# Kernel tuning notes

Measured on AMD Instinct MI355X. Metric: run time of the kernel, lower is better.

## Reference

```python
import jax, jax.numpy as jnp
import numpy as np

N = 50000      # nodes
E = 800000     # edges (avg degree 16)
G = 1024       # graphs in batch
C = 128        # hidden / interaction channels
FIN = 16       # num_node_features
FE = 3         # num_edge_features
L = 3          # num_interactions
CUTOFF = 10.0
LOG2 = float(np.log(2.0))
BN_EPS = 1e-5

def ssp(v):
    # ShiftedSoftplus: softplus(x) - log(2)
    return jax.nn.softplus(v) - LOG2

def setup_inputs() -> dict:
    key = jax.random.key(0)
    ks = jax.random.split(key, 24)
    s = 0.05
    inp = {}
    inp["x"] = jax.random.normal(ks[0], (N, FIN), jnp.float32)
    inp["edge_index"] = jax.random.randint(ks[1], (2, E), 0, N, dtype=jnp.int32)
    inp["edge_weight"] = jax.random.uniform(ks[2], (E,), jnp.float32) * CUTOFF
    inp["edge_attr"] = jax.random.normal(ks[3], (E, FE), jnp.float32)
    inp["batch"] = jnp.sort(jax.random.randint(ks[4], (N,), 0, G, dtype=jnp.int32))
    # node embedding (node_data='x'): Linear(FIN,C) -> Linear(C,C)
    inp["W_l1"] = jax.random.normal(ks[5], (FIN, C), jnp.float32) * s
    inp["b_l1"] = jnp.zeros((C,), jnp.float32)
    inp["W_l2"] = jax.random.normal(ks[6], (C, C), jnp.float32) * s
    inp["b_l2"] = jnp.zeros((C,), jnp.float32)
    # BatchNorm1d affine params
    inp["bn_g"] = jnp.ones((C,), jnp.float32)
    inp["bn_b"] = jnp.zeros((C,), jnp.float32)
    # L stacked interaction layers (SchNet-style CFConv)
    inp["Wi_in"] = jax.random.normal(ks[7], (L, C, C), jnp.float32) * s
    inp["bi_in"] = jnp.zeros((L, C), jnp.float32)
    inp["We1"] = jax.random.normal(ks[8], (L, FE, C), jnp.float32) * s
    inp["be1"] = jnp.zeros((L, C), jnp.float32)
    inp["We2"] = jax.random.normal(ks[9], (L, C, C), jnp.float32) * s
    inp["be2"] = jnp.zeros((L, C), jnp.float32)
    inp["Wi_out"] = jax.random.normal(ks[10], (L, C, C), jnp.float32) * s
    inp["bi_out"] = jnp.zeros((L, C), jnp.float32)
    # GeneralReadOutLayer (128,'sum',32,1): pool -> Linear(128,32)+SSP -> Linear(32,1)+SSP
    inp["W_r1"] = jax.random.normal(ks[11], (C, 32), jnp.float32) * s
    inp["b_r1"] = jnp.zeros((32,), jnp.float32)
    inp["W_r2"] = jax.random.normal(ks[12], (32, 1), jnp.float32) * s
    inp["b_r2"] = jnp.zeros((1,), jnp.float32)
    return inp

def _forward(x, edge_weight, edge_attr,
             W_l1, b_l1, W_l2, b_l2, bn_g, bn_b,
             Wi_in, bi_in, We1, be1, We2, be2, Wi_out, bi_out,
             W_r1, b_r1, W_r2, b_r2, edge_index, batch):
    src, dst = edge_index[0], edge_index[1]
    # node embedding: Linear -> Linear
    h = (x @ W_l1 + b_l1) @ W_l2 + b_l2                   # [N, C]
    # BatchNorm1d (training-mode batch stats over nodes)
    mu = jnp.mean(h, axis=0)
    var = jnp.var(h, axis=0)
    h = (h - mu) * jax.lax.rsqrt(var + BN_EPS) * bn_g + bn_b
    # cosine cutoff envelope on edge distances
    env = 0.5 * (jnp.cos(edge_weight * (jnp.pi / CUTOFF)) + 1.0)  # [E]
    # GeoResNet: residual stack of interactions
    for i in range(L):
        filt = ssp(edge_attr @ We1[i] + be1[i]) @ We2[i] + be2[i]   # [E, C]
        hin = h @ Wi_in[i] + bi_in[i]                               # [N, C]
        msg = hin[src] * filt * env[:, None]                        # [E, C] gather
        agg = jax.ops.segment_sum(msg, dst, num_segments=N)         # [N, C] scatter
        h = h + ssp(agg @ Wi_out[i] + bi_out[i])
    # GeneralReadOutLayer: segment 'sum' pool then MLP with SSP
    hg = jax.ops.segment_sum(h, batch, num_segments=G)              # [G, C]
    out = ssp(hg @ W_r1 + b_r1)
    out = ssp(out @ W_r2 + b_r2)                                    # [G, 1]
    return out.reshape(-1)                                          # [G]

def reference(x, edge_index, edge_weight, edge_attr, batch,
              W_l1, b_l1, W_l2, b_l2, bn_g, bn_b,
              Wi_in, bi_in, We1, be1, We2, be2, Wi_out, bi_out,
              W_r1, b_r1, W_r2, b_r2):
    return _forward(x, edge_weight, edge_attr,
                    W_l1, b_l1, W_l2, b_l2, bn_g, bn_b,
                    Wi_in, bi_in, We1, be1, We2, be2, Wi_out, bi_out,
                    W_r1, b_r1, W_r2, b_r2, edge_index, batch)
```

## Files before the change

kernel.cpp:

```cpp
#include <hip/hip_runtime.h>
#include <hip/hip_bf16.h>
#include <math.h>

#define N_NODES 50000
#define N_EDGES 800000
#define N_GRAPH 1024
#define CDIM 128
#define FINDIM 16
#define NL 3
#define WTP 132
#define NSCB 196

using short8  = __attribute__((ext_vector_type(8))) short;
using floatx4 = __attribute__((ext_vector_type(4))) float;

__device__ __forceinline__ float sspf(float x) {
    return __logf(1.0f + __expf(x)) - 0.6931471805599453f;
}

__device__ __forceinline__ unsigned short f2bf(float f) {
    unsigned int u = __float_as_uint(f);
    u = u + 0x7FFFu + ((u >> 16) & 1u);
    return (unsigned short)(u >> 16);
}

__device__ __forceinline__ float bf2f(unsigned short h) {
    return __uint_as_float((unsigned int)h << 16);
}

__device__ __forceinline__ unsigned int packbf(float a, float b) {
    __hip_bfloat162 h = __float22bfloat162_rn(make_float2(a, b));
    return *(unsigned int*)&h;
}

__device__ __forceinline__ short8 ldfrag(const unsigned short* T, int row, int k0) {
    const uint2* p = (const uint2*)(T + row * WTP + k0);
    short8 r;
    *(uint2*)&r       = p[0];
    *((uint2*)&r + 1) = p[1];
    return r;
}

__global__ void k_fuse(const float* __restrict__ Wl1, const float* __restrict__ bl1,
                       const float* __restrict__ Wl2, const float* __restrict__ bl2,
                       float* __restrict__ Wf, float* __restrict__ bfv) {
    int o = blockIdx.x * 256 + threadIdx.x;
    if (o < FINDIM * CDIM) {
        int f = o >> 7, c = o & 127;
        float s = 0.f;
#pragma unroll 4
        for (int k = 0; k < CDIM; ++k) s += Wl1[f * CDIM + k] * Wl2[k * CDIM + c];
        Wf[o] = s;
    } else if (o < FINDIM * CDIM + CDIM) {
        int c = o - FINDIM * CDIM;
        float s = bl2[c];
#pragma unroll 4
        for (int k = 0; k < CDIM; ++k) s += bl1[k] * Wl2[k * CDIM + c];
        bfv[c] = s;
    }
}

__global__ void k_embed_bn(const float* __restrict__ x, const float* __restrict__ Wf,
                           const float* __restrict__ bfv, float* __restrict__ h,
                           float* __restrict__ bnsum) {
    __shared__ float wfs[FINDIM * CDIM];
    __shared__ float bfs[CDIM];
    __shared__ float sd[512];
    for (int o = threadIdx.x; o < FINDIM * CDIM; o += 256) wfs[o] = Wf[o];
    if (threadIdx.x < CDIM) bfs[threadIdx.x] = bfv[threadIdx.x];
    __syncthreads();
    int c = threadIdx.x & 127;
    int half = threadIdx.x >> 7;
    float s1 = 0.f, s2 = 0.f;
    for (int base = blockIdx.x * 2; base < N_NODES; base += gridDim.x * 2) {
        int n = base + half;
        if (n < N_NODES) {
            float s = bfs[c];
            const float* xp = x + (size_t)n * FINDIM;
#pragma unroll
            for (int f = 0; f < FINDIM; ++f) s += xp[f] * wfs[f * CDIM + c];
            h[(size_t)n * CDIM + c] = s;
            s1 += s; s2 += s * s;
        }
    }
    sd[threadIdx.x] = s1; sd[256 + threadIdx.x] = s2;
    __syncthreads();
    if (threadIdx.x < 128) {
        atomicAdd(&bnsum[threadIdx.x], sd[threadIdx.x] + sd[threadIdx.x + 128]);
        atomicAdd(&bnsum[128 + threadIdx.x], sd[256 + threadIdx.x] + sd[256 + threadIdx.x + 128]);
    }
}

__global__ void k_hist(const int* __restrict__ edst, int* __restrict__ deg) {
    int e = blockIdx.x * 256 + threadIdx.x;
    if (e < N_EDGES) atomicAdd(&deg[edst[e]], 1);
}

__global__ void k_scan1(const int* __restrict__ deg, int* __restrict__ bsum) {
    __shared__ int sd[256];
    int i = blockIdx.x * 256 + threadIdx.x;
    sd[threadIdx.x] = (i < N_NODES) ? deg[i] : 0;
    __syncthreads();
    for (int off = 128; off > 0; off >>= 1) {
        if (threadIdx.x < off) sd[threadIdx.x] += sd[threadIdx.x + off];
        __syncthreads();
    }
    if (threadIdx.x == 0) bsum[blockIdx.x] = sd[0];
}

__global__ void k_scan2(const int* __restrict__ bsum, int* __restrict__ boff,
                        int* __restrict__ row_ptr) {
    __shared__ int sd[256];
    int t = threadIdx.x;
    int v = (t < NSCB) ? bsum[t] : 0;
    sd[t] = v;
    __syncthreads();
    for (int off = 1; off < 256; off <<= 1) {
        int u = (t >= off) ? sd[t - off] : 0;
        __syncthreads();
        sd[t] += u;
        __syncthreads();
    }
    if (t < NSCB) boff[t] = sd[t] - v;
    if (t == 255) row_ptr[N_NODES] = sd[255];
}

__global__ void k_scan3(const int* __restrict__ deg, const int* __restrict__ boff,
                        int* __restrict__ row_ptr) {
    __shared__ int sd[256];
    int i = blockIdx.x * 256 + threadIdx.x;
    int t = threadIdx.x;
    int v = (i < N_NODES) ? deg[i] : 0;
    sd[t] = v;
    __syncthreads();
    for (int off = 1; off < 256; off <<= 1) {
        int u = (t >= off) ? sd[t - off] : 0;
        __syncthreads();
        sd[t] += u;
        __syncthreads();
    }
    if (i < N_NODES) row_ptr[i] = boff[blockIdx.x] + sd[t] - v;
}

__global__ void k_scatter_pack(const int* __restrict__ esrc, const int* __restrict__ edst,
                               const float* __restrict__ ew, const float* __restrict__ ea,
                               const int* __restrict__ row_ptr, int* __restrict__ cnt,
                               int2* __restrict__ rmeta, float4* __restrict__ rea) {
    int e = blockIdx.x * 256 + threadIdx.x;
    if (e < N_EDGES) {
        int d = edst[e];
        int pos = row_ptr[d] + atomicAdd(&cnt[d], 1);
        rmeta[pos] = make_int2(esrc[e], d);
        float w = ew[e];
        float env = 0.5f * (__cosf(w * 0.31415926535897932f) + 1.0f);
        rea[pos] = make_float4(ea[(size_t)e * 3], ea[(size_t)e * 3 + 1],
                               ea[(size_t)e * 3 + 2], env);
    }
}

__global__ __launch_bounds__(256, 2) void k_ngemm_in_bn(float* __restrict__ h,
                                                        const float* __restrict__ bnsum,
                                                        const float* __restrict__ g,
                                                        const float* __restrict__ b,
                                                        const float* __restrict__ B,
                                                        const float* __restrict__ bias,
                                                        unsigned short* __restrict__ hinb) {
    __shared__ unsigned short WT[128 * WTP];
    __shared__ float bs[CDIM];
    __shared__ float scale[CDIM];
    __shared__ float shift[CDIM];
    for (int o = threadIdx.x; o < CDIM * CDIM; o += 256) {
        int k = o >> 7, c = o & 127;
        WT[c * WTP + k] = f2bf(B[o]);
    }
    if (threadIdx.x < CDIM) {
        int c = threadIdx.x;
        const float invN = 1.0f / (float)N_NODES;
        float mu  = bnsum[c] * invN;
        float var = bnsum[128 + c] * invN - mu * mu;
        float sc  = g[c] * rsqrtf(var + 1e-5f);
        scale[c] = sc;
        shift[c] = b[c] - mu * sc;
        bs[c] = bias[c];
    }
    __syncthreads();

    int lane = threadIdx.x & 63, wave = threadIdx.x >> 6;
    int m = lane & 15, q = lane >> 4;
    int rb = blockIdx.x * 64 + wave * 16;
    bool rowok = (rb + m) < N_NODES;
    int row = rowok ? (rb + m) : (N_NODES - 1);

    floatx4 acc[8];
#pragma unroll
    for (int nt = 0; nt < 8; ++nt) acc[nt] = (floatx4){0.f, 0.f, 0.f, 0.f};

#pragma unroll
    for (int kb = 0; kb < 4; ++kb) {
        int k0 = kb * 32 + q * 8;
        float* ap = h + (size_t)row * CDIM + k0;
        float4 lo = *(const float4*)ap;
        float4 hi = *(const float4*)(ap + 4);
        lo.x = fmaf(lo.x, scale[k0 + 0], shift[k0 + 0]);
        lo.y = fmaf(lo.y, scale[k0 + 1], shift[k0 + 1]);
        lo.z = fmaf(lo.z, scale[k0 + 2], shift[k0 + 2]);
        lo.w = fmaf(lo.w, scale[k0 + 3], shift[k0 + 3]);
        hi.x = fmaf(hi.x, scale[k0 + 4], shift[k0 + 4]);
        hi.y = fmaf(hi.y, scale[k0 + 5], shift[k0 + 5]);
        hi.z = fmaf(hi.z, scale[k0 + 6], shift[k0 + 6]);
        hi.w = fmaf(hi.w, scale[k0 + 7], shift[k0 + 7]);
        if (rowok) { *(float4*)ap = lo; *(float4*)(ap + 4) = hi; }
        short8 af;
        ((unsigned int*)&af)[0] = packbf(lo.x, lo.y);
        ((unsigned int*)&af)[1] = packbf(lo.z, lo.w);
        ((unsigned int*)&af)[2] = packbf(hi.x, hi.y);
        ((unsigned int*)&af)[3] = packbf(hi.z, hi.w);
#pragma unroll
        for (int nt = 0; nt < 8; ++nt) {
            short8 bf = ldfrag(WT, nt * 16 + m, k0);
            acc[nt] = __builtin_amdgcn_mfma_f32_16x16x32_bf16(af, bf, acc[nt], 0, 0, 0);
        }
    }
#pragma unroll
    for (int nt = 0; nt < 8; ++nt) {
        int c = nt * 16 + m;
#pragma unroll
        for (int r = 0; r < 4; ++r) {
            int orow = rb + q * 4 + r;
            if (orow < N_NODES)
                hinb[(size_t)orow * CDIM + c] = f2bf(acc[nt][r] + bs[c]);
        }
    }
}

__global__ __launch_bounds__(256, 2) void k_fused_oi(float* __restrict__ agg,
                                                     const float* __restrict__ Bo,
                                                     const float* __restrict__ bo,
                                                     float* __restrict__ h,
                                                     const float* __restrict__ Bi,
                                                     const float* __restrict__ bi,
                                                     unsigned short* __restrict__ hinb) {
    __shared__ unsigned short WT[128 * WTP];
    __shared__ unsigned short hnS[64 * WTP];
    __shared__ float bso[CDIM];
    __shared__ float bsi[CDIM];

    for (int o = threadIdx.x; o < CDIM * CDIM; o += 256) {
        int k = o >> 7, c = o & 127;
        WT[c * WTP + k] = f2bf(Bo[o]);
    }
    if (threadIdx.x < CDIM) { bso[threadIdx.x] = bo[threadIdx.x]; bsi[threadIdx.x] = bi[threadIdx.x]; }
    __syncthreads();

    int lane = threadIdx.x & 63, wave = threadIdx.x >> 6;
    int m = lane & 15, q = lane >> 4;
    int rb = blockIdx.x * 64 + wave * 16;
    int row = rb + m;
    if (row > N_NODES - 1) row = N_NODES - 1;

    floatx4 acc[8];
#pragma unroll
    for (int nt = 0; nt < 8; ++nt) acc[nt] = (floatx4){0.f, 0.f, 0.f, 0.f};

#pragma unroll
    for (int kb = 0; kb < 4; ++kb) {
        int k0 = kb * 32 + q * 8;
        const float* ap = agg + (size_t)row * CDIM + k0;
        float4 lo = *(const float4*)ap;
        float4 hi = *(const float4*)(ap + 4);
        short8 af;
        ((unsigned int*)&af)[0] = packbf(lo.x, lo.y);
        ((unsigned int*)&af)[1] = packbf(lo.z, lo.w);
        ((unsigned int*)&af)[2] = packbf(hi.x, hi.y);
        ((unsigned int*)&af)[3] = packbf(hi.z, hi.w);
#pragma unroll
        for (int nt = 0; nt < 8; ++nt) {
            short8 bf = ldfrag(WT, nt * 16 + m, k0);
            acc[nt] = __builtin_amdgcn_mfma_f32_16x16x32_bf16(af, bf, acc[nt], 0, 0, 0);
        }
    }

#pragma unroll
    for (int nt = 0; nt < 8; ++nt) {
        int c = nt * 16 + m;
#pragma unroll
        for (int r = 0; r < 4; ++r) {
            int lrow = wave * 16 + q * 4 + r;
            int orow = rb + q * 4 + r;
            if (orow < N_NODES) {
                size_t idx = (size_t)orow * CDIM + c;
                float hn = h[idx] + sspf(acc[nt][r] + bso[c]);
                h[idx] = hn;
                agg[idx] = 0.f;
                hnS[lrow * WTP + c] = f2bf(hn);
            } else {
                hnS[lrow * WTP + c] = 0;
            }
        }
    }
    __syncthreads();

    for (int o = threadIdx.x; o < CDIM * CDIM; o += 256) {
        int k = o >> 7, c = o & 127;
        WT[c * WTP + k] = f2bf(Bi[o]);
    }
    __syncthreads();

#pragma unroll
    for (int nt = 0; nt < 8; ++nt) acc[nt] = (floatx4){0.f, 0.f, 0.f, 0.f};
#pragma unroll
    for (int kb = 0; kb < 4; ++kb) {
        int k0 = kb * 32 + q * 8;
        short8 af = ldfrag(hnS, wave * 16 + m, k0);
#pragma unroll
        for (int nt = 0; nt < 8; ++nt) {
            short8 bf = ldfrag(WT, nt * 16 + m, k0);
            acc[nt] = __builtin_amdgcn_mfma_f32_16x16x32_bf16(af, bf, acc[nt], 0, 0, 0);
        }
    }
#pragma unroll
    for (int nt = 0; nt < 8; ++nt) {
        int c = nt * 16 + m;
#pragma unroll
        for (int r = 0; r < 4; ++r) {
            int orow = rb + q * 4 + r;
            if (orow < N_NODES)
                hinb[(size_t)orow * CDIM + c] = f2bf(acc[nt][r] + bsi[c]);
        }
    }
}

__global__ __launch_bounds__(256, 2) void k_ngemm_out_pool(const float* __restrict__ agg,
                                                           const float* __restrict__ B,
                                                           const float* __restrict__ bias,
                                                           const float* __restrict__ h,
                                                           const int* __restrict__ batch,
                                                           float* __restrict__ hg) {
    __shared__ unsigned short WT[128 * WTP];
    __shared__ float bs[CDIM];
    for (int o = threadIdx.x; o < CDIM * CDIM; o += 256) {
        int k = o >> 7, c = o & 127;
        WT[c * WTP + k] = f2bf(B[o]);
    }
    if (threadIdx.x < CDIM) bs[threadIdx.x] = bias[threadIdx.x];
    __syncthreads();

    int lane = threadIdx.x & 63, wave = threadIdx.x >> 6;
    int m = lane & 15, q = lane >> 4;
    int rb = blockIdx.x * 64 + wave * 16;
    int row = rb + m;
    if (row > N_NODES - 1) row = N_NODES - 1;

    floatx4 acc[8];
#pragma unroll
    for (int nt = 0; nt < 8; ++nt) acc[nt] = (floatx4){0.f, 0.f, 0.f, 0.f};

#pragma unroll
    for (int kb = 0; kb < 4; ++kb) {
        int k0 = kb * 32 + q * 8;
        const float* ap = agg + (size_t)row * CDIM + k0;
        float4 lo = *(const float4*)ap;
        float4 hi = *(const float4*)(ap + 4);
        short8 af;
        ((unsigned int*)&af)[0] = packbf(lo.x, lo.y);
        ((unsigned int*)&af)[1] = packbf(lo.z, lo.w);
        ((unsigned int*)&af)[2] = packbf(hi.x, hi.y);
        ((unsigned int*)&af)[3] = packbf(hi.z, hi.w);
#pragma unroll
        for (int nt = 0; nt < 8; ++nt) {
            short8 bf = ldfrag(WT, nt * 16 + m, k0);
            acc[nt] = __builtin_amdgcn_mfma_f32_16x16x32_bf16(af, bf, acc[nt], 0, 0, 0);
        }
    }

    int batchr[4];
#pragma unroll
    for (int r = 0; r < 4; ++r) {
        int orow = rb + q * 4 + r;
        batchr[r] = (orow < N_NODES) ? batch[orow] : 0;
    }
#pragma unroll
    for (int nt = 0; nt < 8; ++nt) {
        int c = nt * 16 + m;
#pragma unroll
        for (int r = 0; r < 4; ++r) {
            int orow = rb + q * 4 + r;
            if (orow < N_NODES) {
                size_t idx = (size_t)orow * CDIM + c;
                float hn = h[idx] + sspf(acc[nt][r] + bs[c]);
                atomicAdd(&hg[(size_t)batchr[r] * CDIM + c], hn);
            }
        }
    }
}

__global__ __launch_bounds__(256, 4) void k_edge(
    const float* __restrict__ We1, const float* __restrict__ be1,
    const float* __restrict__ We2, const float* __restrict__ be2,
    const int2* __restrict__ rmeta, const float4* __restrict__ rea,
    const unsigned short* __restrict__ hin, float* __restrict__ agg) {
    __shared__ unsigned short WT[128 * WTP];
    __shared__ float4 we1i[CDIM];
    __shared__ float  be2s[CDIM];
    __shared__ int2   sds[64];
    __shared__ float4 eas4[64];

    for (int o = threadIdx.x; o < CDIM * CDIM; o += 256) {
        int k = o >> 7, c = o & 127;
        WT[c * WTP + k] = f2bf(We2[o]);
    }
    if (threadIdx.x < CDIM) {
        int k = threadIdx.x;
        we1i[k] = make_float4(We1[k], We1[CDIM + k], We1[2 * CDIM + k], be1[k]);
        be2s[k] = be2[k];
    }
    __syncthreads();

    int lane = threadIdx.x & 63, wave = threadIdx.x >> 6;
    int m = lane & 15, q = lane >> 4;

    float biasr[8];
#pragma unroll
    for (int nt = 0; nt < 8; ++nt) biasr[nt] = be2s[nt * 16 + m];

    const int ntiles = N_EDGES / 64;
    int tpb = (ntiles + gridDim.x - 1) / gridDim.x;
    int t0 = blockIdx.x * tpb;
    int t1 = t0 + tpb; if (t1 > ntiles) t1 = ntiles;

    for (int tile = t0; tile < t1; ++tile) {
        int s0 = tile * 64;
        __syncthreads();
        if (threadIdx.x < 64)       sds[threadIdx.x]       = rmeta[s0 + threadIdx.x];
        else if (threadIdx.x < 128) eas4[threadIdx.x - 64] = rea[s0 + threadIdx.x - 64];
        __syncthreads();

        int el0 = wave * 16 + q * 4;
        int2 sd[4]; float ev[4];
#pragma unroll
        for (int r = 0; r < 4; ++r) { sd[r] = sds[el0 + r]; ev[r] = eas4[el0 + r].w; }

        unsigned short hpre[4][8];
#pragma unroll
        for (int r = 0; r < 4; ++r) {
            const unsigned short* hp = hin + (size_t)sd[r].x * CDIM + m;
#pragma unroll
            for (int nt = 0; nt < 8; ++nt) hpre[r][nt] = hp[nt * 16];
        }

        float4 eav = eas4[wave * 16 + m];
        float ea0 = eav.x, ea1 = eav.y, ea2 = eav.z;
        short8 af[4];
#pragma unroll
        for (int kb = 0; kb < 4; ++kb) {
#pragma unroll
            for (int jj = 0; jj < 4; ++jj) {
                int k = kb * 32 + q * 8 + jj * 2;
                float4 w0 = we1i[k];
                float4 w1 = we1i[k + 1];
                float p0 = fmaf(w0.x, ea0, fmaf(w0.y, ea1, fmaf(w0.z, ea2, w0.w)));
                float p1 = fmaf(w1.x, ea0, fmaf(w1.y, ea1, fmaf(w1.z, ea2, w1.w)));
                ((unsigned int*)&af[kb])[jj] = packbf(sspf(p0), sspf(p1));
            }
        }

        floatx4 acc[8];
#pragma unroll
        for (int nt = 0; nt < 8; ++nt)
            acc[nt] = (floatx4){biasr[nt], biasr[nt], biasr[nt], biasr[nt]};
#pragma unroll
        for (int kb = 0; kb < 4; ++kb)
#pragma unroll
            for (int nt = 0; nt < 8; ++nt) {
                short8 bf = ldfrag(WT, nt * 16 + m, kb * 32 + q * 8);
                acc[nt] = __builtin_amdgcn_mfma_f32_16x16x32_bf16(af[kb], bf, acc[nt], 0, 0, 0);
            }

        bool uni = (sd[0].y == sd[3].y);
        float vv[8];
#pragma unroll
        for (int nt = 0; nt < 8; ++nt) {
            float s = 0.f;
#pragma unroll
            for (int r = 0; r < 4; ++r)
                s += acc[nt][r] * ev[r] * bf2f(hpre[r][nt]);
            vv[nt] = s;
        }

        int owner = uni ? 1 : 0;
        int myd   = uni ? sd[0].y : -1 - lane;
#pragma unroll
        for (int s = 16; s <= 32; s <<= 1) {
            int od = __shfl_xor(myd, s, 64);
            int oo = __shfl_xor(owner, s, 64);
            bool match = owner && oo && (od == myd);
            bool lower = ((lane & s) == 0);
#pragma unroll
            for (int nt = 0; nt < 8; ++nt) {
                float ovv = __shfl_xor(vv[nt], s, 64);
                if (match && lower) vv[nt] += ovv;
            }
            if (match && !lower) { owner = 0; myd = -1 - lane; }
        }

        if (uni) {
            if (owner) {
                float* ap = agg + (size_t)myd * CDIM + m;
#pragma unroll
                for (int nt = 0; nt < 8; ++nt) atomicAdd(&ap[nt * 16], vv[nt]);
            }
        } else {
#pragma unroll
            for (int nt = 0; nt < 8; ++nt) {
                int c = nt * 16 + m;
                int cur = sd[0].y;
                float accv = acc[nt][0] * ev[0] * bf2f(hpre[0][nt]);
#pragma unroll
                for (int r = 1; r < 4; ++r) {
                    float msg = acc[nt][r] * ev[r] * bf2f(hpre[r][nt]);
                    if (sd[r].y != cur) {
                        atomicAdd(&agg[(size_t)cur * CDIM + c], accv);
                        cur = sd[r].y; accv = msg;
                    } else {
                        accv += msg;
                    }
                }
                atomicAdd(&agg[(size_t)cur * CDIM + c], accv);
            }
        }
    }
}

__global__ void k_readout(const float* __restrict__ hg, const float* __restrict__ Wr1,
                          const float* __restrict__ br1, const float* __restrict__ Wr2,
                          const float* __restrict__ br2, float* __restrict__ out) {
    __shared__ float hgs[CDIM];
    int g = blockIdx.x;
    for (int o = threadIdx.x; o < CDIM; o += 64) hgs[o] = hg[(size_t)g * CDIM + o];
    __syncthreads();
    int c = threadIdx.x;
    float val = 0.f;
    if (c < 32) {
        float s = br1[c];
        for (int k = 0; k < CDIM; ++k) s += hgs[k] * Wr1[k * 32 + c];
        val = sspf(s) * Wr2[c];
    }
#pragma unroll
    for (int off = 16; off >= 1; off >>= 1) val += __shfl_down(val, off, 32);
    if (c == 0) out[g] = sspf(val + br2[0]);
}

extern "C" void kernel_launch(void* const* d_in, const int* in_sizes, int n_in,
                              void* d_out, int out_size, void* d_ws, size_t ws_size,
                              hipStream_t stream) {
    const float* x     = (const float*)d_in[0];
    const int*   eidx  = (const int*)  d_in[1];
    const float* ew    = (const float*)d_in[2];
    const float* ea    = (const float*)d_in[3];
    const int*   batch = (const int*)  d_in[4];
    const float* Wl1   = (const float*)d_in[5];
    const float* bl1   = (const float*)d_in[6];
    const float* Wl2   = (const float*)d_in[7];
    const float* bl2   = (const float*)d_in[8];
    const float* bng   = (const float*)d_in[9];
    const float* bnb   = (const float*)d_in[10];
    const float* Wi_in = (const float*)d_in[11];
    const float* bi_in = (const float*)d_in[12];
    const float* We1   = (const float*)d_in[13];
    const float* be1   = (const float*)d_in[14];
    const float* We2   = (const float*)d_in[15];
    const float* be2   = (const float*)d_in[16];
    const float* Wi_o  = (const float*)d_in[17];
    const float* bi_o  = (const float*)d_in[18];
    const float* Wr1   = (const float*)d_in[19];
    const float* br1   = (const float*)d_in[20];
    const float* Wr2   = (const float*)d_in[21];
    const float* br2   = (const float*)d_in[22];
    float* out = (float*)d_out;

    float* ws  = (float*)d_ws;
    float*  h    = ws;
    float*  agg  = h + (size_t)N_NODES * CDIM;
    float4* rea  = (float4*)(agg + (size_t)N_NODES * CDIM);
    float*  hg   = (float*)(rea + N_EDGES);
    float*  Wf   = hg + (size_t)N_GRAPH * CDIM;
    float*  bfv  = Wf + FINDIM * CDIM;
    float*  bnsum = bfv + CDIM;
    unsigned short* hinb = (unsigned short*)(bnsum + 256);
    int2*  rmeta  = (int2*)(hinb + (size_t)N_NODES * CDIM);
    int*   deg    = (int*)(rmeta + N_EDGES);
    int*   row_ptr= deg + N_NODES;
    int*   cnt    = row_ptr + N_NODES + 1;
    int*   bsum   = cnt + N_NODES;
    int*   boff   = bsum + NSCB;

    const int* esrc = eidx;
    const int* edst = eidx + N_EDGES;

    hipMemsetAsync(deg, 0, (size_t)N_NODES * sizeof(int), stream);
    hipMemsetAsync(cnt, 0, (size_t)N_NODES * sizeof(int), stream);
    k_hist<<<(N_EDGES + 255) / 256, 256, 0, stream>>>(edst, deg);
    k_scan1<<<NSCB, 256, 0, stream>>>(deg, bsum);
    k_scan2<<<1, 256, 0, stream>>>(bsum, boff, row_ptr);
    k_scan3<<<NSCB, 256, 0, stream>>>(deg, boff, row_ptr);
    k_scatter_pack<<<(N_EDGES + 255) / 256, 256, 0, stream>>>(esrc, edst, ew, ea,
                                                              row_ptr, cnt, rmeta, rea);

    hipMemsetAsync(bnsum, 0, 256 * sizeof(float), stream);
    k_fuse<<<9, 256, 0, stream>>>(Wl1, bl1, Wl2, bl2, Wf, bfv);
    k_embed_bn<<<512, 256, 0, stream>>>(x, Wf, bfv, h, bnsum);

    hipMemsetAsync(agg, 0, (size_t)N_NODES * CDIM * sizeof(float), stream);
    hipMemsetAsync(hg, 0, (size_t)N_GRAPH * CDIM * sizeof(float), stream);
    const int ngrid = (N_NODES + 63) / 64;

    k_ngemm_in_bn<<<ngrid, 256, 0, stream>>>(h, bnsum, bng, bnb, Wi_in, bi_in, hinb);
    for (int l = 0; l < NL; ++l) {
        k_edge<<<1024, 256, 0, stream>>>(We1 + l * 3 * CDIM, be1 + l * CDIM,
                                         We2 + (size_t)l * CDIM * CDIM, be2 + l * CDIM,
                                         rmeta, rea, hinb, agg);
        if (l < NL - 1)
            k_fused_oi<<<ngrid, 256, 0, stream>>>(agg, Wi_o + (size_t)l * CDIM * CDIM,
                                                  bi_o + l * CDIM, h,
                                                  Wi_in + (size_t)(l + 1) * CDIM * CDIM,
                                                  bi_in + (l + 1) * CDIM, hinb);
        else
            k_ngemm_out_pool<<<ngrid, 256, 0, stream>>>(agg, Wi_o + (size_t)l * CDIM * CDIM,
                                                        bi_o + l * CDIM, h, batch, hg);
    }

    k_readout<<<N_GRAPH, 64, 0, stream>>>(hg, Wr1, br1, Wr2, br2, out);
}
```

Baseline: 861.4 us.

## Permute bf16 hin layout for vector gathers, merge scan and memset launches

The bf16 hin buffer is now written channel-interleaved, so each lane stores and later gathers 8 contiguous values with one 16-byte access instead of 8 strided 2-byte accesses in the edge kernel. The three-pass prefix scan is replaced by a single decoupled-lookback scan that uses a ticket counter and per-block flags. The separate weight-fusion kernel is folded into the embedding kernel, where every block recomputes the fused weights. The workspace is reordered so all zero-initialised buffers are cleared with one memset. Risks are the redundant per-block weight products in the embedding kernel and serial spin-waiting in the lookback scan.

```diff
diff --git a/kernel.cpp b/kernel.cpp
--- a/kernel.cpp
+++ b/kernel.cpp
@@ -41,33 +41,28 @@
     return r;
 }
 
-__global__ void k_fuse(const float* __restrict__ Wl1, const float* __restrict__ bl1,
-                       const float* __restrict__ Wl2, const float* __restrict__ bl2,
-                       float* __restrict__ Wf, float* __restrict__ bfv) {
-    int o = blockIdx.x * 256 + threadIdx.x;
-    if (o < FINDIM * CDIM) {
+
+__global__ void k_embed_bn(const float* __restrict__ x,
+                           const float* __restrict__ Wl1, const float* __restrict__ bl1,
+                           const float* __restrict__ Wl2, const float* __restrict__ bl2,
+                           float* __restrict__ h, float* __restrict__ bnsum) {
+    __shared__ float wfs[FINDIM * CDIM];
+    __shared__ float bfs[CDIM];
+    __shared__ float sd[512];
+    for (int o = threadIdx.x; o < FINDIM * CDIM; o += 256) {
         int f = o >> 7, c = o & 127;
         float s = 0.f;
 #pragma unroll 4
         for (int k = 0; k < CDIM; ++k) s += Wl1[f * CDIM + k] * Wl2[k * CDIM + c];
-        Wf[o] = s;
-    } else if (o < FINDIM * CDIM + CDIM) {
-        int c = o - FINDIM * CDIM;
+        wfs[o] = s;
+    }
+    if (threadIdx.x < CDIM) {
+        int c = threadIdx.x;
         float s = bl2[c];
 #pragma unroll 4
         for (int k = 0; k < CDIM; ++k) s += bl1[k] * Wl2[k * CDIM + c];
-        bfv[c] = s;
-    }
-}
-
-__global__ void k_embed_bn(const float* __restrict__ x, const float* __restrict__ Wf,
-                           const float* __restrict__ bfv, float* __restrict__ h,
-                           float* __restrict__ bnsum) {
-    __shared__ float wfs[FINDIM * CDIM];
-    __shared__ float bfs[CDIM];
-    __shared__ float sd[512];
-    for (int o = threadIdx.x; o < FINDIM * CDIM; o += 256) wfs[o] = Wf[o];
-    if (threadIdx.x < CDIM) bfs[threadIdx.x] = bfv[threadIdx.x];
+        bfs[c] = s;
+    }
     __syncthreads();
     int c = threadIdx.x & 127;
     int half = threadIdx.x >> 7;
@@ -96,23 +91,17 @@
     if (e < N_EDGES) atomicAdd(&deg[edst[e]], 1);
 }
 
-__global__ void k_scan1(const int* __restrict__ deg, int* __restrict__ bsum) {
+__global__ void k_scan_dl(const int* __restrict__ deg, int* __restrict__ row_ptr,
+                          int* __restrict__ ticket, int* __restrict__ pval,
+                          int* __restrict__ pflg) {
     __shared__ int sd[256];
-    int i = blockIdx.x * 256 + threadIdx.x;
-    sd[threadIdx.x] = (i < N_NODES) ? deg[i] : 0;
-    __syncthreads();
-    for (int off = 128; off > 0; off >>= 1) {
-        if (threadIdx.x < off) sd[threadIdx.x] += sd[threadIdx.x + off];
-        __syncthreads();
-    }
-    if (threadIdx.x == 0) bsum[blockIdx.x] = sd[0];
-}
-
-__global__ void k_scan2(const int* __restrict__ bsum, int* __restrict__ boff,
-                        int* __restrict__ row_ptr) {
-    __shared__ int sd[256];
+    __shared__ int bid_s, pref_s;
     int t = threadIdx.x;
-    int v = (t < NSCB) ? bsum[t] : 0;
+    if (t == 0) bid_s = atomicAdd(ticket, 1);
+    __syncthreads();
+    int bid = bid_s;
+    int i = bid * 256 + t;
+    int v = (i < N_NODES) ? deg[i] : 0;
     sd[t] = v;
     __syncthreads();
     for (int off = 1; off < 256; off <<= 1) {
@@ -121,25 +110,28 @@
         sd[t] += u;
         __syncthreads();
     }
-    if (t < NSCB) boff[t] = sd[t] - v;
-    if (t == 255) row_ptr[N_NODES] = sd[255];
-}
-
-__global__ void k_scan3(const int* __restrict__ deg, const int* __restrict__ boff,
-                        int* __restrict__ row_ptr) {
-    __shared__ int sd[256];
-    int i = blockIdx.x * 256 + threadIdx.x;
-    int t = threadIdx.x;
-    int v = (i < N_NODES) ? deg[i] : 0;
-    sd[t] = v;
-    __syncthreads();
-    for (int off = 1; off < 256; off <<= 1) {
-        int u = (t >= off) ? sd[t - off] : 0;
-        __syncthreads();
-        sd[t] += u;
-        __syncthreads();
-    }
-    if (i < N_NODES) row_ptr[i] = boff[blockIdx.x] + sd[t] - v;
+    if (t == 0) {
+        int total = sd[255];
+        atomicExch(&pval[2 * bid], total);
+        __threadfence();
+        atomicExch(&pflg[2 * bid], 1);
+        int ex = 0;
+        for (int p = bid - 1; p >= 0; --p) {
+            int fi, fa;
+            do {
+                fi = atomicOr(&pflg[2 * p + 1], 0);
+                fa = atomicOr(&pflg[2 * p], 0);
+            } while (fi == 0 && fa == 0);
+            if (fi) { ex += atomicOr(&pval[2 * p + 1], 0); break; }
+            ex += atomicOr(&pval[2 * p], 0);
+        }
+        atomicExch(&pval[2 * bid + 1], ex + total);
+        __threadfence();
+        atomicExch(&pflg[2 * bid + 1], 1);
+        pref_s = ex;
+    }
+    __syncthreads();
+    if (i < N_NODES) row_ptr[i] = pref_s + sd[t] - v;
 }
 
 __global__ void k_scatter_pack(const int* __restrict__ esrc, const int* __restrict__ edst,
@@ -222,13 +214,15 @@
         }
     }
 #pragma unroll
-    for (int nt = 0; nt < 8; ++nt) {
-        int c = nt * 16 + m;
-#pragma unroll
-        for (int r = 0; r < 4; ++r) {
-            int orow = rb + q * 4 + r;
-            if (orow < N_NODES)
-                hinb[(size_t)orow * CDIM + c] = f2bf(acc[nt][r] + bs[c]);
+    for (int r = 0; r < 4; ++r) {
+        int orow = rb + q * 4 + r;
+        if (orow < N_NODES) {
+            short8 o8;
+#pragma unroll
+            for (int j = 0; j < 4; ++j)
+                ((unsigned int*)&o8)[j] = packbf(acc[2 * j][r] + bs[(2 * j) * 16 + m],
+                                                 acc[2 * j + 1][r] + bs[(2 * j + 1) * 16 + m]);
+            *(short8*)(hinb + (size_t)orow * CDIM + m * 8) = o8;
         }
     }
 }
@@ -319,13 +313,15 @@
         }
     }
 #pragma unroll
-    for (int nt = 0; nt < 8; ++nt) {
-        int c = nt * 16 + m;
-#pragma unroll
-        for (int r = 0; r < 4; ++r) {
-            int orow = rb + q * 4 + r;
-            if (orow < N_NODES)
-                hinb[(size_t)orow * CDIM + c] = f2bf(acc[nt][r] + bsi[c]);
+    for (int r = 0; r < 4; ++r) {
+        int orow = rb + q * 4 + r;
+        if (orow < N_NODES) {
+            short8 o8;
+#pragma unroll
+            for (int j = 0; j < 4; ++j)
+                ((unsigned int*)&o8)[j] = packbf(acc[2 * j][r] + bsi[(2 * j) * 16 + m],
+                                                 acc[2 * j + 1][r] + bsi[(2 * j + 1) * 16 + m]);
+            *(short8*)(hinb + (size_t)orow * CDIM + m * 8) = o8;
         }
     }
 }
@@ -440,13 +436,10 @@
 #pragma unroll
         for (int r = 0; r < 4; ++r) { sd[r] = sds[el0 + r]; ev[r] = eas4[el0 + r].w; }
 
-        unsigned short hpre[4][8];
-#pragma unroll
-        for (int r = 0; r < 4; ++r) {
-            const unsigned short* hp = hin + (size_t)sd[r].x * CDIM + m;
-#pragma unroll
-            for (int nt = 0; nt < 8; ++nt) hpre[r][nt] = hp[nt * 16];
-        }
+        short8 hpre[4];
+#pragma unroll
+        for (int r = 0; r < 4; ++r)
+            hpre[r] = *(const short8*)(hin + (size_t)sd[r].x * CDIM + m * 8);
 
         float4 eav = eas4[wave * 16 + m];
         float ea0 = eav.x, ea1 = eav.y, ea2 = eav.z;
@@ -483,7 +476,7 @@
             float s = 0.f;
 #pragma unroll
             for (int r = 0; r < 4; ++r)
-                s += acc[nt][r] * ev[r] * bf2f(hpre[r][nt]);
+                s += acc[nt][r] * ev[r] * bf2f((unsigned short)hpre[r][nt]);
             vv[nt] = s;
         }
 
@@ -514,10 +507,10 @@
             for (int nt = 0; nt < 8; ++nt) {
                 int c = nt * 16 + m;
                 int cur = sd[0].y;
-                float accv = acc[nt][0] * ev[0] * bf2f(hpre[0][nt]);
+                float accv = acc[nt][0] * ev[0] * bf2f((unsigned short)hpre[0][nt]);
 #pragma unroll
                 for (int r = 1; r < 4; ++r) {
-                    float msg = acc[nt][r] * ev[r] * bf2f(hpre[r][nt]);
+                    float msg = acc[nt][r] * ev[r] * bf2f((unsigned short)hpre[r][nt]);
                     if (sd[r].y != cur) {
                         atomicAdd(&agg[(size_t)cur * CDIM + c], accv);
                         cur = sd[r].y; accv = msg;
@@ -579,41 +572,34 @@
     float* out = (float*)d_out;
 
     float* ws  = (float*)d_ws;
-    float*  h    = ws;
-    float*  agg  = h + (size_t)N_NODES * CDIM;
-    float4* rea  = (float4*)(agg + (size_t)N_NODES * CDIM);
-    float*  hg   = (float*)(rea + N_EDGES);
-    float*  Wf   = hg + (size_t)N_GRAPH * CDIM;
-    float*  bfv  = Wf + FINDIM * CDIM;
-    float*  bnsum = bfv + CDIM;
-    unsigned short* hinb = (unsigned short*)(bnsum + 256);
+    float*  h     = ws;
+    float4* rea   = (float4*)(h + (size_t)N_NODES * CDIM);
+    unsigned short* hinb = (unsigned short*)(rea + N_EDGES);
     int2*  rmeta  = (int2*)(hinb + (size_t)N_NODES * CDIM);
-    int*   deg    = (int*)(rmeta + N_EDGES);
-    int*   row_ptr= deg + N_NODES;
-    int*   cnt    = row_ptr + N_NODES + 1;
-    int*   bsum   = cnt + N_NODES;
-    int*   boff   = bsum + NSCB;
+    int*   row_ptr= (int*)(rmeta + N_EDGES);
+    float* agg    = (float*)(row_ptr + ((N_NODES + 15) & ~15));
+    float* hg     = agg + (size_t)N_NODES * CDIM;
+    float* bnsum  = hg + (size_t)N_GRAPH * CDIM;
+    int*   deg    = (int*)(bnsum + 256);
+    int*   cnt    = deg + N_NODES;
+    int*   ticket = cnt + N_NODES;
+    int*   pval   = ticket + 4;
+    int*   pflg   = pval + 2 * NSCB;
+    size_t zbytes = (size_t)((char*)(pflg + 2 * NSCB) - (char*)agg);
 
     const int* esrc = eidx;
     const int* edst = eidx + N_EDGES;
 
-    hipMemsetAsync(deg, 0, (size_t)N_NODES * sizeof(int), stream);
-    hipMemsetAsync(cnt, 0, (size_t)N_NODES * sizeof(int), stream);
+    hipMemsetAsync(agg, 0, zbytes, stream);
+
     k_hist<<<(N_EDGES + 255) / 256, 256, 0, stream>>>(edst, deg);
-    k_scan1<<<NSCB, 256, 0, stream>>>(deg, bsum);
-    k_scan2<<<1, 256, 0, stream>>>(bsum, boff, row_ptr);
-    k_scan3<<<NSCB, 256, 0, stream>>>(deg, boff, row_ptr);
+    k_scan_dl<<<NSCB, 256, 0, stream>>>(deg, row_ptr, ticket, pval, pflg);
     k_scatter_pack<<<(N_EDGES + 255) / 256, 256, 0, stream>>>(esrc, edst, ew, ea,
                                                               row_ptr, cnt, rmeta, rea);
 
-    hipMemsetAsync(bnsum, 0, 256 * sizeof(float), stream);
-    k_fuse<<<9, 256, 0, stream>>>(Wl1, bl1, Wl2, bl2, Wf, bfv);
-    k_embed_bn<<<512, 256, 0, stream>>>(x, Wf, bfv, h, bnsum);
-
-    hipMemsetAsync(agg, 0, (size_t)N_NODES * CDIM * sizeof(float), stream);
-    hipMemsetAsync(hg, 0, (size_t)N_GRAPH * CDIM * sizeof(float), stream);
+    k_embed_bn<<<512, 256, 0, stream>>>(x, Wl1, bl1, Wl2, bl2, h, bnsum);
+
     const int ngrid = (N_NODES + 63) / 64;
-
     k_ngemm_in_bn<<<ngrid, 256, 0, stream>>>(h, bnsum, bng, bnb, Wi_in, bi_in, hinb);
     for (int l = 0; l < NL; ++l) {
         k_edge<<<1024, 256, 0, stream>>>(We1 + l * 3 * CDIM, be1 + l * CDIM,
```

Result: slower. 903.5 us (+4.9%).
